# Performance work log

Measured on AMD Instinct MI355X. Metric: run time of the kernel, lower is better.

## Reference

```python
import jax, jax.numpy as jnp
import numpy as np

B, C, H, W = 16, 64, 128, 128
C8 = C // 8


def setup_inputs() -> dict:
    key = jax.random.key(0)
    ks = jax.random.split(key, 8)
    s = 0.05
    return {
        "x": jax.random.normal(ks[0], (B, C, H, W), dtype=jnp.float32),
        "Wq": jax.random.normal(ks[1], (C8, C), dtype=jnp.float32) * s,
        "bq": jax.random.normal(ks[2], (C8,), dtype=jnp.float32) * s,
        "Wk": jax.random.normal(ks[3], (C8, C), dtype=jnp.float32) * s,
        "bk": jax.random.normal(ks[4], (C8,), dtype=jnp.float32) * s,
        "Wv": jax.random.normal(ks[5], (C, C), dtype=jnp.float32) * s,
        "bv": jax.random.normal(ks[6], (C,), dtype=jnp.float32) * s,
        "gamma": jnp.zeros((1,), dtype=jnp.float32),
    }


def _criss_cross(x, Wq, bq, Wk, bk, Wv, bv, gamma):
    # 1x1 convs == channel-mixing matmuls
    q = jnp.einsum("bchw,oc->bohw", x, Wq) + bq[None, :, None, None]  # [B,C8,H,W]
    k = jnp.einsum("bchw,oc->bohw", x, Wk) + bk[None, :, None, None]  # [B,C8,H,W]
    v = jnp.einsum("bchw,oc->bohw", x, Wv) + bv[None, :, None, None]  # [B,C,H,W]

    h = x.shape[2]
    # column (H-axis) attention scores; diagonal masked to -inf
    energy_H = jnp.einsum("bchw,bciw->bhwi", q, k)  # [B,H,W,H]
    diag = jnp.eye(h, dtype=bool)[None, :, None, :]  # mask where query row == key row
    energy_H = jnp.where(diag, -jnp.inf, energy_H)
    # row (W-axis) attention scores
    energy_W = jnp.einsum("bchw,bchj->bhwj", q, k)  # [B,H,W,W]

    # joint softmax over concatenated H+W axis
    att = jax.nn.softmax(jnp.concatenate([energy_H, energy_W], axis=3), axis=3)
    att_H = att[:, :, :, :h]    # [B,H,W,H]
    att_W = att[:, :, :, h:]    # [B,H,W,W]

    out_H = jnp.einsum("bhwi,bciw->bchw", att_H, v)
    out_W = jnp.einsum("bhwj,bchj->bchw", att_W, v)
    return gamma[0] * (out_H + out_W) + x


def reference(x, Wq, bq, Wk, bk, Wv, bv, gamma):
    return _criss_cross(x, Wq, bq, Wk, bk, Wv, bv, gamma)
```

## Files before the change

### kernel.cpp

```cpp
#include <hip/hip_runtime.h>

#define HW 128
#define CC 64
#define C8V 8
#define NB 16

typedef _Float16 h1;
typedef _Float16 h2 __attribute__((ext_vector_type(2)));
typedef _Float16 half8 __attribute__((ext_vector_type(8)));
typedef float float16v __attribute__((ext_vector_type(16)));
typedef uint uv4 __attribute__((ext_vector_type(4)));

__device__ __forceinline__ uint packh2(float a, float b) {
#if __has_builtin(__builtin_amdgcn_cvt_pkrtz)
  return __builtin_bit_cast(uint, __builtin_amdgcn_cvt_pkrtz(a, b));
#else
  h2 v; v[0] = (h1)a; v[1] = (h1)b; return __builtin_bit_cast(uint, v);
#endif
}
__device__ __forceinline__ ushort f2h(float a) { h1 v = (h1)a; return __builtin_bit_cast(ushort, v); }
__device__ __forceinline__ float  h2f(ushort a) { return (float)__builtin_bit_cast(h1, a); }

__device__ __forceinline__ float16v mfma16(uv4 a, uv4 b, float16v c) {
  return __builtin_amdgcn_mfma_f32_32x32x16_f16(
      __builtin_bit_cast(half8, a), __builtin_bit_cast(half8, b), c, 0, 0, 0);
}

__global__ __launch_bounds__(256) void k_proj(
    const float* __restrict__ x,
    const float* __restrict__ Wq, const float* __restrict__ bq,
    const float* __restrict__ Wk, const float* __restrict__ bk,
    const float* __restrict__ Wv, const float* __restrict__ bv,
    ushort* __restrict__ q, ushort* __restrict__ k, ushort* __restrict__ v)
{
  alignas(16) __shared__ ushort smem[16128];
  __shared__ float bias_l[96];
  ushort* x_l = smem;
  ushort* W_l = smem + 128 * 72;

  int t = threadIdx.x;
  int lane = t & 63, wv = t >> 6;
  int b = blockIdx.x >> 7, r = blockIdx.x & 127;

  #pragma unroll
  for (int i = 0; i < 20; ++i) {
    int idx = t + 256 * i; int o_ = idx >> 6, c = idx & 63;
    float wval = (o_ < 8) ? Wq[o_ * 64 + c] : (o_ < 16) ? Wk[(o_ - 8) * 64 + c] : Wv[(o_ - 16) * 64 + c];
    W_l[o_ * 72 + c] = f2h(wval);
  }
  if (t < 96) bias_l[t] = (t < 8) ? bq[t] : (t < 16) ? bk[t - 8] : (t < 80) ? bv[t - 16] : 0.f;

  const float* xrow = x + (size_t)(b * CC) * (HW * HW) + (size_t)r * HW;
  #pragma unroll
  for (int i = 0; i < 8; ++i) {
    int idx = t + 256 * i; int c = idx >> 5, w4 = idx & 31;
    float4 xv = *(const float4*)(xrow + (size_t)c * (HW * HW) + w4 * 4);
    x_l[(w4 * 4 + 0) * 72 + c] = f2h(xv.x);
    x_l[(w4 * 4 + 1) * 72 + c] = f2h(xv.y);
    x_l[(w4 * 4 + 2) * 72 + c] = f2h(xv.z);
    x_l[(w4 * 4 + 3) * 72 + c] = f2h(xv.w);
  }
  __syncthreads();

  int w = 32 * wv + (lane & 31);
  float16v acc0 = {}, acc1 = {}, acc2 = {};
  #pragma unroll
  for (int ks = 0; ks < 4; ++ks) {
    int c0 = 8 * (lane >> 5) + 16 * ks;
    uv4 Bx = *(const uv4*)&x_l[w * 72 + c0];
    uv4 a0 = *(const uv4*)&W_l[((lane & 31) + 0) * 72 + c0];
    uv4 a1 = *(const uv4*)&W_l[((lane & 31) + 32) * 72 + c0];
    uv4 a2 = *(const uv4*)&W_l[((lane & 31) + 64) * 72 + c0];
    acc0 = mfma16(a0, Bx, acc0);
    acc1 = mfma16(a1, Bx, acc1);
    acc2 = mfma16(a2, Bx, acc2);
  }
  __syncthreads();

  ushort* o_l = smem;
  int hi = lane >> 5;
  #pragma unroll
  for (int reg = 0; reg < 16; ++reg) {
    int orow = (reg & 3) + 8 * (reg >> 2) + 4 * hi;
    o_l[(orow +  0) * 128 + w] = f2h(acc0[reg] + bias_l[orow]);
    o_l[(orow + 32) * 128 + w] = f2h(acc1[reg] + bias_l[orow + 32]);
    if (orow + 64 < 80)
      o_l[(orow + 64) * 128 + w] = f2h(acc2[reg] + bias_l[orow + 64]);
  }
  __syncthreads();

  ushort* qb = q + (size_t)(b * C8V) * (HW * HW) + (size_t)r * HW;
  ushort* kb = k + (size_t)(b * C8V) * (HW * HW) + (size_t)r * HW;
  ushort* vb = v + (size_t)(b * CC)  * (HW * HW) + (size_t)r * HW;
  #pragma unroll
  for (int i = 0; i < 5; ++i) {
    int idx = t + 256 * i; int o_ = idx >> 4, w8 = idx & 15;
    uv4 val = *(const uv4*)&o_l[o_ * 128 + w8 * 8];
    ushort* dst = (o_ < 8) ? qb + (size_t)o_ * (HW * HW)
                : (o_ < 16) ? kb + (size_t)(o_ - 8) * (HW * HW)
                            : vb + (size_t)(o_ - 16) * (HW * HW);
    *(uv4*)(dst + w8 * 8) = val;
  }
}

__global__ __launch_bounds__(256) void k_transpose_all(
    const ushort* __restrict__ q, ushort* __restrict__ qT,
    const ushort* __restrict__ k, ushort* __restrict__ kT,
    const ushort* __restrict__ v, ushort* __restrict__ vT)
{
  __shared__ ushort tl[128 * 130];
  int t = threadIdx.x;
  int p = blockIdx.x;
  const ushort* in; ushort* out;
  if (p < 128)      { size_t base = (size_t)p * (HW * HW);         in = q + base; out = qT + base; }
  else if (p < 256) { size_t base = (size_t)(p - 128) * (HW * HW); in = k + base; out = kT + base; }
  else              { size_t base = (size_t)(p - 256) * (HW * HW); in = v + base; out = vT + base; }
  const uint* ip = (const uint*)in;
  uint* op = (uint*)out;
  int c2 = t & 63;
  int r0 = t >> 6;
  for (int it = 0; it < 32; ++it) {
    int r = it * 4 + r0;
    uint val = ip[r * 64 + c2];
    *(uint*)&tl[r * 130 + c2 * 2] = val;
  }
  __syncthreads();
  for (int it = 0; it < 32; ++it) {
    int wcol = it * 4 + r0;
    int hh = c2 * 2;
    uint lo = tl[hh * 130 + wcol];
    uint hi = tl[(hh + 1) * 130 + wcol];
    op[wcol * 64 + c2] = lo | (hi << 16);
  }
}

__global__ __launch_bounds__(256) void k_attn_both(
    const ushort* __restrict__ q,  const ushort* __restrict__ kkn, const ushort* __restrict__ vn,
    const ushort* __restrict__ qT, const ushort* __restrict__ kkT, const ushort* __restrict__ vT,
    ushort* __restrict__ oW_, float* __restrict__ mW_, float* __restrict__ sW_,
    ushort* __restrict__ oH_, float* __restrict__ mH_, float* __restrict__ sH_)
{
  alignas(16) __shared__ ushort Q_l[128][16];
  alignas(16) __shared__ ushort K_l[128][16];
  alignas(16) __shared__ uint   V_l[64 * 64];

  int t = threadIdx.x;
  int lane = t & 63, wv = t >> 6;
  int hi = lane >> 5;
  int bid = blockIdx.x & 2047;
  bool maskf = blockIdx.x >= 2048;
  const ushort* qp = maskf ? qT : q;
  const ushort* kp = maskf ? kkT : kkn;
  const ushort* vp = maskf ? vT : vn;
  ushort* op = maskf ? oH_ : oW_;
  float* mo = maskf ? mH_ : mW_;
  float* so = maskf ? sH_ : sW_;

  int b = bid >> 7, r = bid & 127;
  size_t plane32 = (size_t)(HW * HW) / 2;

  if (t < 128) {
    *(uv4*)&Q_l[t][8] = (uv4){0, 0, 0, 0};
    *(uv4*)&K_l[t][8] = (uv4){0, 0, 0, 0};
  }
  const uint* qrow = (const uint*)qp + (size_t)(b * C8V) * plane32 + (size_t)r * 64;
  const uint* krow = (const uint*)kp + (size_t)(b * C8V) * plane32 + (size_t)r * 64;
  #pragma unroll
  for (int i = 0; i < 2; ++i) {
    int idx = t + 256 * i; int c = idx >> 6, w2 = idx & 63;
    uint qv = qrow[(size_t)c * plane32 + w2];
    Q_l[2 * w2][c] = (ushort)(qv & 0xffff); Q_l[2 * w2 + 1][c] = (ushort)(qv >> 16);
    uint kv = krow[(size_t)c * plane32 + w2];
    K_l[2 * w2][c] = (ushort)(kv & 0xffff); K_l[2 * w2 + 1][c] = (ushort)(kv >> 16);
  }
  const uint* vrow = (const uint*)vp + (size_t)(b * CC) * plane32 + (size_t)r * 64;
  #pragma unroll
  for (int i = 0; i < 16; ++i) {
    int idx = t + 256 * i; int c = idx >> 6, j2 = idx & 63;
    uint val = vrow[(size_t)c * plane32 + j2];
    uint byteoff = c * 256 + ((4 * j2) ^ ((c & 15) << 4));
    V_l[byteoff >> 2] = val;
  }
  __syncthreads();

  uv4 Bq = *(const uv4*)&Q_l[(lane & 31) + 32 * wv][hi * 8];
  float16v e[4];
  #pragma unroll
  for (int mt = 0; mt < 4; ++mt) {
    uv4 ka = *(const uv4*)&K_l[(lane & 31) + 32 * mt][hi * 8];
    float16v z = {};
    e[mt] = mfma16(ka, Bq, z);
  }

  int qg = 32 * wv + (lane & 31);
  float m = -INFINITY;
  #pragma unroll
  for (int mt = 0; mt < 4; ++mt) {
    #pragma unroll
    for (int reg = 0; reg < 16; ++reg) {
      float ev = e[mt][reg];
      if (maskf) {
        int key = 32 * mt + ((reg & 3) + 8 * (reg >> 2) + 4 * hi);
        ev = (key == qg) ? -INFINITY : ev;
        e[mt][reg] = ev;
      }
      m = fmaxf(m, ev);
    }
  }
  m = fmaxf(m, __shfl_xor(m, 32));
  float s = 0.f;
  #pragma unroll
  for (int mt = 0; mt < 4; ++mt) {
    #pragma unroll
    for (int reg = 0; reg < 16; ++reg) {
      float p = __expf(e[mt][reg] - m);
      e[mt][reg] = p;
      s += p;
    }
  }
  s += __shfl_xor(s, 32);
  if (lane < 32) {
    mo[(size_t)bid * HW + qg] = m;
    so[(size_t)bid * HW + qg] = s;
  }

  float16v acc0 = {}, acc1 = {};
  #pragma unroll
  for (int s8 = 0; s8 < 8; ++s8) {
    int mt = s8 >> 1, hf = s8 & 1;
    float p0 = e[mt][8 * hf + 0], p1 = e[mt][8 * hf + 1];
    float p2 = e[mt][8 * hf + 2], p3 = e[mt][8 * hf + 3];
    float p4 = e[mt][8 * hf + 4], p5 = e[mt][8 * hf + 5];
    float p6 = e[mt][8 * hf + 6], p7 = e[mt][8 * hf + 7];
    uint X = packh2(p0, p1), Y = packh2(p2, p3), Z = packh2(p4, p5), Wp = packh2(p6, p7);
    uint Xs = __shfl_xor(X, 32), Ys = __shfl_xor(Y, 32);
    uint Zs = __shfl_xor(Z, 32), Ws = __shfl_xor(Wp, 32);
    uv4 Bp;
    Bp[0] = (hi == 0) ? X  : Zs;
    Bp[1] = (hi == 0) ? Y  : Ws;
    Bp[2] = (hi == 0) ? Xs : Z;
    Bp[3] = (hi == 0) ? Ys : Wp;
    #pragma unroll
    for (int ct = 0; ct < 2; ++ct) {
      int c = (lane & 31) + 32 * ct;
      uint byteoff = c * 256 + ((16 * (hi + 2 * s8)) ^ ((c & 15) << 4));
      uv4 va = *(const uv4*)((const char*)V_l + byteoff);
      if (ct == 0) acc0 = mfma16(va, Bp, acc0);
      else         acc1 = mfma16(va, Bp, acc1);
    }
  }

  __syncthreads();
  ushort* o_l = (ushort*)V_l;
  int w = 32 * wv + (lane & 31);
  #pragma unroll
  for (int reg = 0; reg < 16; ++reg) {
    int c = (reg & 3) + 8 * (reg >> 2) + 4 * hi;
    o_l[(c +  0) * 128 + w] = f2h(acc0[reg]);
    o_l[(c + 32) * 128 + w] = f2h(acc1[reg]);
  }
  __syncthreads();
  ushort* ob = op + (size_t)(b * CC) * (HW * HW) + (size_t)r * HW;
  #pragma unroll
  for (int i = 0; i < 4; ++i) {
    int idx = t + 256 * i; int c = idx >> 4, w8 = idx & 15;
    *(uv4*)(ob + (size_t)c * (HW * HW) + w8 * 8) = *(const uv4*)&o_l[c * 128 + w8 * 8];
  }
}

__global__ __launch_bounds__(256) void k_merge(
    const ushort* __restrict__ oHT, const ushort* __restrict__ oW,
    const float* __restrict__ mH, const float* __restrict__ sH,
    const float* __restrict__ mW, const float* __restrict__ sW,
    const float* __restrict__ x, const float* __restrict__ gamma,
    float* __restrict__ out)
{
  __shared__ float aH_l[32 * 129];
  __shared__ float aW_l[128 * 36];
  alignas(16) __shared__ ushort otile[4 * 32 * 132];
  float* tmpM = (float*)otile;
  float* tmpS = tmpM + 32 * 129;

  int t = threadIdx.x;
  int bid = blockIdx.x;
  int wsel = bid & 3, cg = (bid >> 2) & 15, b = bid >> 6;
  int w0 = wsel * 32;
  float g = gamma[0];
  const int PL = HW * HW;
  const float* mHb = mH + (size_t)b * PL;
  const float* sHb = sH + (size_t)b * PL;
  const float* mWb = mW + (size_t)b * PL;
  const float* sWb = sW + (size_t)b * PL;

  #pragma unroll
  for (int i = 0; i < 16; ++i) {
    int p = t + 256 * i; int h = p & 127, w = p >> 7;
    tmpM[w * 129 + h] = mHb[(w0 + w) * HW + h];
    tmpS[w * 129 + h] = sHb[(w0 + w) * HW + h];
  }
  __syncthreads();
  #pragma unroll
  for (int i = 0; i < 16; ++i) {
    int p = t + 256 * i; int w = p & 31, h = p >> 5;
    float mw = mWb[h * HW + w0 + w], sw = sWb[h * HW + w0 + w];
    float mh = tmpM[w * 129 + h],    sh = tmpS[w * 129 + h];
    float mm = fmaxf(mh, mw);
    float eh = __expf(mh - mm), ew = __expf(mw - mm);
    float inv = 1.f / (sh * eh + sw * ew);
    aH_l[w * 129 + h] = eh * inv;
    aW_l[h * 36 + w]  = ew * inv;
  }
  __syncthreads();

  #pragma unroll
  for (int i = 0; i < 8; ++i) {
    int p = t + 256 * i;
    int ch = p >> 9, rest = p & 511;
    int w = rest >> 4, hg = rest & 15;
    size_t cbase = (size_t)(b * CC + cg * 4 + ch) * PL;
    uv4 ov = *(const uv4*)(oHT + cbase + (size_t)(w0 + w) * HW + hg * 8);
    const float* ah = &aH_l[w * 129 + hg * 8];
    uint res[4];
    #pragma unroll
    for (int jj = 0; jj < 4; ++jj) {
      float lo = h2f((ushort)(ov[jj] & 0xffff)) * ah[2 * jj];
      float hi = h2f((ushort)(ov[jj] >> 16))    * ah[2 * jj + 1];
      res[jj] = packh2(lo, hi);
    }
    ushort* dst = &otile[(ch * 32 + w) * 132 + hg * 8];
    *(uint2*)dst       = make_uint2(res[0], res[1]);
    *(uint2*)(dst + 4) = make_uint2(res[2], res[3]);
  }
  __syncthreads();

  #pragma unroll
  for (int ch = 0; ch < 4; ++ch) {
    size_t cbase = (size_t)(b * CC + cg * 4 + ch) * PL;
    const ushort* otc = &otile[ch * 32 * 132];
    #pragma unroll
    for (int i = 0; i < 2; ++i) {
      int p = t + 256 * i;
      int w4 = p & 7, h2 = p >> 3;
      float th0[4], th1[4];
      #pragma unroll
      for (int j = 0; j < 4; ++j) {
        uint pk = *(const uint*)&otc[(4 * w4 + j) * 132 + 2 * h2];
        th0[j] = h2f((ushort)(pk & 0xffff));
        th1[j] = h2f((ushort)(pk >> 16));
      }
      #pragma unroll
      for (int rr = 0; rr < 2; ++rr) {
        int hh = 2 * h2 + rr;
        const float* th = rr ? th1 : th0;
        size_t base = cbase + (size_t)hh * HW + w0 + 4 * w4;
        float4 aw = *(const float4*)&aW_l[hh * 36 + 4 * w4];
        uint2 ow2 = *(const uint2*)(oW + base);
        float4 xv = *(const float4*)(x + base);
        float4 res;
        res.x = g * (th[0] + h2f((ushort)(ow2.x & 0xffff)) * aw.x) + xv.x;
        res.y = g * (th[1] + h2f((ushort)(ow2.x >> 16))    * aw.y) + xv.y;
        res.z = g * (th[2] + h2f((ushort)(ow2.y & 0xffff)) * aw.z) + xv.z;
        res.w = g * (th[3] + h2f((ushort)(ow2.y >> 16))    * aw.w) + xv.w;
        *(float4*)(out + base) = res;
      }
    }
  }
}

extern "C" void kernel_launch(void* const* d_in, const int* in_sizes, int n_in,
                              void* d_out, int out_size, void* d_ws, size_t ws_size,
                              hipStream_t stream)
{
  const float* x     = (const float*)d_in[0];
  const float* Wq    = (const float*)d_in[1];
  const float* bq    = (const float*)d_in[2];
  const float* Wk    = (const float*)d_in[3];
  const float* bk    = (const float*)d_in[4];
  const float* Wv    = (const float*)d_in[5];
  const float* bv    = (const float*)d_in[6];
  const float* gamma = (const float*)d_in[7];
  float* out = (float*)d_out;

  char* w = (char*)d_ws;
  size_t np = (size_t)NB * HW * HW;
  ushort* q   = (ushort*)w;  w += np * C8V * 2;
  ushort* k   = (ushort*)w;  w += np * C8V * 2;
  ushort* qT  = (ushort*)w;  w += np * C8V * 2;
  ushort* kT  = (ushort*)w;  w += np * C8V * 2;
  ushort* v   = (ushort*)w;  w += np * CC * 2;
  ushort* vT  = (ushort*)w;  w += np * CC * 2;
  ushort* oW  = (ushort*)w;  w += np * CC * 2;
  ushort* oHT = (ushort*)w;  w += np * CC * 2;
  float* mW = (float*)w;  w += np * 4;
  float* sW = (float*)w;  w += np * 4;
  float* mH = (float*)w;  w += np * 4;
  float* sH = (float*)w;  w += np * 4;
  if ((size_t)(w - (char*)d_ws) > ws_size) return;

  k_proj<<<NB * HW, 256, 0, stream>>>(x, Wq, bq, Wk, bk, Wv, bv, q, k, v);
  k_transpose_all<<<256 + NB * CC, 256, 0, stream>>>(q, qT, k, kT, v, vT);
  k_attn_both<<<2 * NB * HW, 256, 0, stream>>>(q, k, v, qT, kT, vT,
                                               oW, mW, sW, oHT, mH, sH);
  k_merge<<<NB * 16 * 4, 256, 0, stream>>>(oHT, oW, mH, sH, mW, sW, x, gamma, out);
}
```

Measured before the change: 123.9 us.

## Precompute softmax merge coefficients once in separate fp16 kernel

Adds a k_alpha kernel that computes the H/W softmax combination weights once per pixel and stores them in fp16 (aH transposed, aW normal layout). k_merge previously recomputed these from fp32 max/sum buffers in every channel-group block, causing 16x redundant reads and exp work. The merge now loads fp16 weights and uses packed half multiplies. It costs an extra launch and reduces weight precision to fp16.

```diff
diff --git a/kernel.cpp b/kernel.cpp
--- a/kernel.cpp
+++ b/kernel.cpp
@@ -268,49 +268,61 @@
   }
 }
 
+__global__ __launch_bounds__(256) void k_alpha(
+    const float* __restrict__ mH, const float* __restrict__ sH,
+    const float* __restrict__ mW, const float* __restrict__ sW,
+    ushort* __restrict__ aHT, ushort* __restrict__ aWn)
+{
+  __shared__ float mw_l[128 * 17], sw_l[128 * 17];
+  __shared__ ushort aw_l[128 * 18];
+  int t = threadIdx.x;
+  int b = blockIdx.x >> 3, ws = blockIdx.x & 7;
+  int w0 = ws * 16;
+  const int PL = HW * HW;
+
+  #pragma unroll
+  for (int i = 0; i < 8; ++i) {
+    int p = t + 256 * i;
+    int w = p & 15, h = p >> 4;
+    mw_l[h * 17 + w] = mW[(size_t)b * PL + h * HW + w0 + w];
+    sw_l[h * 17 + w] = sW[(size_t)b * PL + h * HW + w0 + w];
+  }
+  __syncthreads();
+  #pragma unroll
+  for (int i = 0; i < 8; ++i) {
+    int p = t + 256 * i;
+    int h = p & 127, w = p >> 7;
+    size_t tidx = (size_t)b * PL + (size_t)(w0 + w) * HW + h;
+    float mh = mH[tidx], sh = sH[tidx];
+    float mw = mw_l[h * 17 + w], sw = sw_l[h * 17 + w];
+    float mm = fmaxf(mh, mw);
+    float eh = __expf(mh - mm), ew = __expf(mw - mm);
+    float inv = 1.f / (sh * eh + sw * ew);
+    aHT[tidx] = f2h(eh * inv);
+    aw_l[h * 18 + w] = f2h(ew * inv);
+  }
+  __syncthreads();
+  #pragma unroll
+  for (int i = 0; i < 8; ++i) {
+    int p = t + 256 * i;
+    int w = p & 15, h = p >> 4;
+    aWn[(size_t)b * PL + (size_t)h * HW + w0 + w] = aw_l[h * 18 + w];
+  }
+}
+
 __global__ __launch_bounds__(256) void k_merge(
     const ushort* __restrict__ oHT, const ushort* __restrict__ oW,
-    const float* __restrict__ mH, const float* __restrict__ sH,
-    const float* __restrict__ mW, const float* __restrict__ sW,
+    const ushort* __restrict__ aHT, const ushort* __restrict__ aWn,
     const float* __restrict__ x, const float* __restrict__ gamma,
     float* __restrict__ out)
 {
-  __shared__ float aH_l[32 * 129];
-  __shared__ float aW_l[128 * 36];
   alignas(16) __shared__ ushort otile[4 * 32 * 132];
-  float* tmpM = (float*)otile;
-  float* tmpS = tmpM + 32 * 129;
-
   int t = threadIdx.x;
   int bid = blockIdx.x;
   int wsel = bid & 3, cg = (bid >> 2) & 15, b = bid >> 6;
   int w0 = wsel * 32;
   float g = gamma[0];
   const int PL = HW * HW;
-  const float* mHb = mH + (size_t)b * PL;
-  const float* sHb = sH + (size_t)b * PL;
-  const float* mWb = mW + (size_t)b * PL;
-  const float* sWb = sW + (size_t)b * PL;
-
-  #pragma unroll
-  for (int i = 0; i < 16; ++i) {
-    int p = t + 256 * i; int h = p & 127, w = p >> 7;
-    tmpM[w * 129 + h] = mHb[(w0 + w) * HW + h];
-    tmpS[w * 129 + h] = sHb[(w0 + w) * HW + h];
-  }
-  __syncthreads();
-  #pragma unroll
-  for (int i = 0; i < 16; ++i) {
-    int p = t + 256 * i; int w = p & 31, h = p >> 5;
-    float mw = mWb[h * HW + w0 + w], sw = sWb[h * HW + w0 + w];
-    float mh = tmpM[w * 129 + h],    sh = tmpS[w * 129 + h];
-    float mm = fmaxf(mh, mw);
-    float eh = __expf(mh - mm), ew = __expf(mw - mm);
-    float inv = 1.f / (sh * eh + sw * ew);
-    aH_l[w * 129 + h] = eh * inv;
-    aW_l[h * 36 + w]  = ew * inv;
-  }
-  __syncthreads();
 
   #pragma unroll
   for (int i = 0; i < 8; ++i) {
@@ -319,17 +331,15 @@
     int w = rest >> 4, hg = rest & 15;
     size_t cbase = (size_t)(b * CC + cg * 4 + ch) * PL;
     uv4 ov = *(const uv4*)(oHT + cbase + (size_t)(w0 + w) * HW + hg * 8);
-    const float* ah = &aH_l[w * 129 + hg * 8];
-    uint res[4];
+    uv4 av = *(const uv4*)(aHT + (size_t)b * PL + (size_t)(w0 + w) * HW + hg * 8);
+    uv4 res;
     #pragma unroll
     for (int jj = 0; jj < 4; ++jj) {
-      float lo = h2f((ushort)(ov[jj] & 0xffff)) * ah[2 * jj];
-      float hi = h2f((ushort)(ov[jj] >> 16))    * ah[2 * jj + 1];
-      res[jj] = packh2(lo, hi);
+      h2 o2 = __builtin_bit_cast(h2, ov[jj]);
+      h2 a2 = __builtin_bit_cast(h2, av[jj]);
+      res[jj] = __builtin_bit_cast(uint, o2 * a2);
     }
-    ushort* dst = &otile[(ch * 32 + w) * 132 + hg * 8];
-    *(uint2*)dst       = make_uint2(res[0], res[1]);
-    *(uint2*)(dst + 4) = make_uint2(res[2], res[3]);
+    *(uv4*)&otile[(ch * 32 + w) * 132 + hg * 8] = res;
   }
   __syncthreads();
 
@@ -340,27 +350,28 @@
     #pragma unroll
     for (int i = 0; i < 2; ++i) {
       int p = t + 256 * i;
-      int w4 = p & 7, h2 = p >> 3;
+      int w4 = p & 7, hh2 = p >> 3;
       float th0[4], th1[4];
       #pragma unroll
       for (int j = 0; j < 4; ++j) {
-        uint pk = *(const uint*)&otc[(4 * w4 + j) * 132 + 2 * h2];
+        uint pk = *(const uint*)&otc[(4 * w4 + j) * 132 + 2 * hh2];
         th0[j] = h2f((ushort)(pk & 0xffff));
         th1[j] = h2f((ushort)(pk >> 16));
       }
       #pragma unroll
       for (int rr = 0; rr < 2; ++rr) {
-        int hh = 2 * h2 + rr;
+        int hh = 2 * hh2 + rr;
         const float* th = rr ? th1 : th0;
         size_t base = cbase + (size_t)hh * HW + w0 + 4 * w4;
-        float4 aw = *(const float4*)&aW_l[hh * 36 + 4 * w4];
+        size_t abase = (size_t)b * PL + (size_t)hh * HW + w0 + 4 * w4;
+        uint2 aw2 = *(const uint2*)(aWn + abase);
         uint2 ow2 = *(const uint2*)(oW + base);
         float4 xv = *(const float4*)(x + base);
         float4 res;
-        res.x = g * (th[0] + h2f((ushort)(ow2.x & 0xffff)) * aw.x) + xv.x;
-        res.y = g * (th[1] + h2f((ushort)(ow2.x >> 16))    * aw.y) + xv.y;
-        res.z = g * (th[2] + h2f((ushort)(ow2.y & 0xffff)) * aw.z) + xv.z;
-        res.w = g * (th[3] + h2f((ushort)(ow2.y >> 16))    * aw.w) + xv.w;
+        res.x = g * (th[0] + h2f((ushort)(ow2.x & 0xffff)) * h2f((ushort)(aw2.x & 0xffff))) + xv.x;
+        res.y = g * (th[1] + h2f((ushort)(ow2.x >> 16))    * h2f((ushort)(aw2.x >> 16)))    + xv.y;
+        res.z = g * (th[2] + h2f((ushort)(ow2.y & 0xffff)) * h2f((ushort)(aw2.y & 0xffff))) + xv.z;
+        res.w = g * (th[3] + h2f((ushort)(ow2.y >> 16))    * h2f((ushort)(aw2.y >> 16)))    + xv.w;
         *(float4*)(out + base) = res;
       }
     }
@@ -395,11 +406,14 @@
   float* sW = (float*)w;  w += np * 4;
   float* mH = (float*)w;  w += np * 4;
   float* sH = (float*)w;  w += np * 4;
+  ushort* aHT = (ushort*)w; w += np * 2;
+  ushort* aWn = (ushort*)w; w += np * 2;
   if ((size_t)(w - (char*)d_ws) > ws_size) return;
 
   k_proj<<<NB * HW, 256, 0, stream>>>(x, Wq, bq, Wk, bk, Wv, bv, q, k, v);
   k_transpose_all<<<256 + NB * CC, 256, 0, stream>>>(q, qT, k, kT, v, vT);
   k_attn_both<<<2 * NB * HW, 256, 0, stream>>>(q, k, v, qT, kT, vT,
                                                oW, mW, sW, oHT, mH, sH);
-  k_merge<<<NB * 16 * 4, 256, 0, stream>>>(oHT, oW, mH, sH, mW, sW, x, gamma, out);
-}
+  k_alpha<<<NB * 8, 256, 0, stream>>>(mH, sH, mW, sW, aHT, aWn);
+  k_merge<<<NB * 16 * 4, 256, 0, stream>>>(oHT, oW, aHT, aWn, x, gamma, out);
+}
```

Measured after the change: 123.9 us. No clear change (+0.0%).
